# Kernel tuning notes

Hardware: AMD Instinct MI355X
Metric: run time of the kernel (lower is better)

## Reference

```python
import jax, jax.numpy as jnp
import numpy as np

N = 50000
E = 800000
IN_C, HID, OUT_C, DEPTH, HEADS = 3, 128, 64, 4, 4
EPS = 1e-6
NEG_SLOPE = 0.2  # PyG GATConv default leaky_relu slope


def setup_inputs() -> dict:
    key = jax.random.key(0)
    ks = jax.random.split(key, 12)
    x = jax.random.normal(ks[0], (N, IN_C), dtype=jnp.float32)
    edge_index = jax.random.randint(ks[1], (2, E), 0, N, dtype=jnp.int32)
    s = 0.05
    return {
        "x": x,
        "edge_index": edge_index,
        "W_in": jax.random.normal(ks[2], (IN_C, HID), dtype=jnp.float32) * s,
        "b_in": jnp.zeros((HID,), jnp.float32),
        # per-layer GATConv params, stacked over depth
        "W_conv": jax.random.normal(ks[3], (DEPTH, HID, HEADS * HID), dtype=jnp.float32) * s,
        "att_src": jax.random.normal(ks[4], (DEPTH, HEADS, HID), dtype=jnp.float32) * s,
        "att_dst": jax.random.normal(ks[5], (DEPTH, HEADS, HID), dtype=jnp.float32) * s,
        "b_conv": jnp.zeros((DEPTH, HID), jnp.float32),
        "ln_gamma": jnp.ones((DEPTH, HID), jnp.float32),
        "ln_beta": jnp.zeros((DEPTH, HID), jnp.float32),
        "W_out": jax.random.normal(ks[6], (HID, OUT_C), dtype=jnp.float32) * s,
        "b_out": jnp.zeros((OUT_C,), jnp.float32),
    }


def _layer_norm(x, gamma, beta):
    mu = jnp.mean(x, axis=-1, keepdims=True)
    var = jnp.mean(jnp.square(x - mu), axis=-1, keepdims=True)
    return (x - mu) * jax.lax.rsqrt(var + EPS) * gamma + beta


def _gat_conv(x, src, dst, W, a_src, a_dst, bias):
    # x: [N, HID]; src/dst: [E2] (self-loops already appended)
    xh = (x @ W).reshape(N, HEADS, HID)                       # [N, H, C]
    alpha_s = jnp.einsum("nhc,hc->nh", xh, a_src)             # [N, H]
    alpha_d = jnp.einsum("nhc,hc->nh", xh, a_dst)             # [N, H]
    e = jax.nn.leaky_relu(alpha_s[src] + alpha_d[dst], NEG_SLOPE)  # [E2, H]
    # segment softmax over incoming edges of each destination node
    m = jax.ops.segment_max(e, dst, num_segments=N)           # [N, H]
    p = jnp.exp(e - m[dst])                                   # [E2, H]
    z = jax.ops.segment_sum(p, dst, num_segments=N)           # [N, H]
    alpha = p / z[dst]                                        # [E2, H]
    msg = alpha[:, :, None] * xh[src]                         # [E2, H, C]
    out = jax.ops.segment_sum(msg, dst, num_segments=N)       # [N, H, C]
    # concat=False -> mean over heads, then bias
    return out.mean(axis=1) + bias


def reference(x, edge_index, W_in, b_in, W_conv, att_src, att_dst, b_conv,
              ln_gamma, ln_beta, W_out, b_out):
    # add self-loops (PyG GATConv default add_self_loops=True)
    loops = jnp.arange(N, dtype=edge_index.dtype)
    src = jnp.concatenate([edge_index[0], loops])
    dst = jnp.concatenate([edge_index[1], loops])

    h = x @ W_in + b_in
    for i in range(DEPTH):
        residual = h
        h = _layer_norm(h, ln_gamma[i], ln_beta[i])
        h = _gat_conv(h, src, dst, W_conv[i], att_src[i], att_dst[i], b_conv[i])
        h = jax.nn.relu(h)
        h = h + residual
    return h @ W_out + b_out
```

## Files before the change

### kernel.cpp

```cpp
#include <hip/hip_runtime.h>
#include <hip/hip_fp16.h>
#include <math.h>

#define N_NODES 50000
#define E_EDGES 800000
#define E2 (E_EDGES + N_NODES)
#define HID 128
#define HEADS 4
#define OUTC 64
#define DEPTH 4
#define NEG_SLOPE 0.2f
#define LN_EPS 1e-6f
#define NT2 3125
#define AROW 520

typedef float f32x4 __attribute__((ext_vector_type(4)));
typedef float f32x2 __attribute__((ext_vector_type(2)));
typedef _Float16 half8 __attribute__((ext_vector_type(8)));


__global__ void k_deg(const int* __restrict__ ei, int* __restrict__ deg) {
    int e = blockIdx.x * 256 + threadIdx.x;
    if (e >= E2) return;
    int d = (e < E_EDGES) ? ei[E_EDGES + e] : (e - E_EDGES);
    atomicAdd(&deg[d], 1);
}


__global__ __launch_bounds__(256) void k_hist(const int* __restrict__ deg,
                                              int* __restrict__ hist) {
    __shared__ int lh[256];
    int t = threadIdx.x;
    lh[t] = 0;
    __syncthreads();
    int base = blockIdx.x * 1024;
    #pragma unroll
    for (int i = 0; i < 4; ++i) {
        int n = base + t + i * 256;
        if (n < N_NODES) atomicAdd(&lh[min(deg[n], 255)], 1);
    }
    __syncthreads();
    if (lh[t]) atomicAdd(&hist[t], lh[t]);
}


__global__ void k_hscan(const int* __restrict__ hist, int* __restrict__ hcur,
                        int* __restrict__ nprefix, int* __restrict__ eprefix,
                        int* __restrict__ row_ptr) {
    __shared__ int sm[256], se[256];
    int t = threadIdx.x;
    int v = hist[t];
    sm[t] = v;
    se[t] = v * t;
    __syncthreads();
    for (int off = 1; off < 256; off <<= 1) {
        int u = (t >= off) ? sm[t - off] : 0;
        int w = (t >= off) ? se[t - off] : 0;
        __syncthreads();
        sm[t] += u;
        se[t] += w;
        __syncthreads();
    }
    int np = sm[t] - v;
    int ep = se[t] - v * t;
    hcur[t] = np;
    nprefix[t] = np;
    eprefix[t] = ep;
    if (t == 0) row_ptr[N_NODES] = E2;
}


__global__ __launch_bounds__(256) void k_permfill(const int* __restrict__ deg,
                                                  int* __restrict__ hcur,
                                                  const int* __restrict__ nprefix,
                                                  const int* __restrict__ eprefix,
                                                  int* __restrict__ perm,
                                                  int* __restrict__ inv,
                                                  int* __restrict__ row_ptr) {
    __shared__ int lh[256];
    __shared__ int lbase[256];
    int t = threadIdx.x;
    lh[t] = 0;
    __syncthreads();
    int base = blockIdx.x * 1024;
    int myb[4], myr[4];
    #pragma unroll
    for (int i = 0; i < 4; ++i) {
        int n = base + t + i * 256;
        if (n < N_NODES) {
            int b = min(deg[n], 255);
            myb[i] = b;
            myr[i] = atomicAdd(&lh[b], 1);
        } else myb[i] = -1;
    }
    __syncthreads();
    if (lh[t]) lbase[t] = atomicAdd(&hcur[t], lh[t]);
    __syncthreads();
    #pragma unroll
    for (int i = 0; i < 4; ++i) {
        if (myb[i] >= 0) {
            int n = base + t + i * 256;
            int b = myb[i];
            int pos = lbase[b] + myr[i];
            perm[pos] = n;
            inv[n] = pos;
            row_ptr[pos] = eprefix[b] + (pos - nprefix[b]) * b;
        }
    }
}

__global__ void k_fill(const int* __restrict__ ei, const int* __restrict__ row_ptr,
                       const int* __restrict__ inv, int* __restrict__ cur,
                       int* __restrict__ csr_src) {
    int e = blockIdx.x * 256 + threadIdx.x;
    if (e >= E2) return;
    int s, d;
    if (e < E_EDGES) { s = ei[e]; d = ei[E_EDGES + e]; } else { s = d = e - E_EDGES; }
    int nd = inv[d], ns = inv[s];
    int pos = atomicAdd(&cur[nd], 1);
    csr_src[row_ptr[nd] + pos] = ns;
}


__global__ void k_prep(const float* __restrict__ W_conv, const float* __restrict__ att_s,
                       const float* __restrict__ att_d, const float* __restrict__ W_out,
                       _Float16* __restrict__ Bp, float* __restrict__ ws_all,
                       _Float16* __restrict__ Bout) {
    int idx = blockIdx.x * 256 + threadIdx.x;
    if (idx < DEPTH * 65536) {
        int jj    = idx & 7;
        int lane  = (idx >> 3) & 63;
        int kc    = (idx >> 9) & 15;
        int ntile = (idx >> 13) & 7;
        int layer = idx >> 16;
        int k = kc * 32 + (lane >> 4) * 8 + jj;
        int n = ntile * 16 + (lane & 15);
        int hh = k >> 7;
        int s  = k & 127;
        int c  = (s & 7) * 16 + (s >> 3);
        Bp[idx] = (_Float16)(0.25f * W_conv[(size_t)layer * 65536 + (size_t)c * 512 + hh * HID + n]);
        return;
    }
    int i2 = idx - DEPTH * 65536;
    if (i2 < DEPTH * 1024) {
        int j = i2 & 7, c = (i2 >> 3) & 127, layer = i2 >> 10;
        int hh = j & 3, sd = j >> 2;
        const float* Wr = W_conv + (size_t)layer * 65536 + (size_t)c * 512 + hh * HID;
        const float* at = (sd ? att_d : att_s) + (size_t)layer * HEADS * HID + hh * HID;
        float s = 0.f;
        for (int cc = 0; cc < HID; ++cc) s += Wr[cc] * at[cc];
        ws_all[i2] = s;
        return;
    }
    int i3 = i2 - DEPTH * 1024;
    if (i3 < 8192) {
        int j    = i3 & 7;
        int lane = (i3 >> 3) & 63;
        int nt   = (i3 >> 9) & 3;
        int kc   = i3 >> 11;
        int k = kc * 32 + (lane >> 4) * 8 + j;
        int c = (k & 7) * 16 + (k >> 3);
        int n = nt * 16 + (lane & 15);
        Bout[i3] = (_Float16)W_out[(size_t)c * OUTC + n];
    }
}


__global__ __launch_bounds__(256) void k_in_proj_ln(const float* __restrict__ x,
                                                    const int* __restrict__ perm,
                                                    const float* __restrict__ W,
                                                    const float* __restrict__ bias,
                                                    const float* __restrict__ gamma,
                                                    const float* __restrict__ beta,
                                                    const float* __restrict__ ws,
                                                    float* __restrict__ h,
                                                    unsigned char* __restrict__ ln8,
                                                    float* __restrict__ as_,
                                                    float* __restrict__ ad_) {
    int tid = threadIdx.x;
    int lane = tid & 63;
    int nd = blockIdx.x * 4 + (tid >> 6);
    int orig = perm[nd];
    const float* xr = x + (size_t)orig * 3;
    float x0 = xr[0], x1 = xr[1], x2 = xr[2];
    int j0 = lane, j1 = lane + 64;
    float a = bias[j0] + x0 * W[j0] + x1 * W[HID + j0] + x2 * W[2 * HID + j0];
    float b = bias[j1] + x0 * W[j1] + x1 * W[HID + j1] + x2 * W[2 * HID + j1];
    size_t base = (size_t)nd * HID;
    h[base + j0] = a;
    h[base + j1] = b;
    float s = a + b;
    for (int o = 1; o < 64; o <<= 1) s += __shfl_xor(s, o);
    float mu = s * (1.0f / 128.0f);
    float da = a - mu, db = b - mu;
    float v = da * da + db * db;
    for (int o = 1; o < 64; o <<= 1) v += __shfl_xor(v, o);
    float rstd = rsqrtf(v * (1.0f / 128.0f) + LN_EPS);
    float va = da * rstd * gamma[j0] + beta[j0];
    float vb = db * rstd * gamma[j1] + beta[j1];

    float ap[8];
    for (int j = 0; j < 8; ++j)
        ap[j] = va * ws[j0 * 8 + j] + vb * ws[j1 * 8 + j];
    for (int o = 1; o < 64; o <<= 1)
        for (int j = 0; j < 8; ++j) ap[j] += __shfl_xor(ap[j], o);
    if (lane == 0) {
        for (int hh = 0; hh < 4; ++hh) {
            as_[nd * 4 + hh] = ap[hh];
            ad_[nd * 4 + hh] = ap[4 + hh];
        }
    }

    float pv[8];
    for (int t = 0; t < 8; ++t) {
        int c = t * 16 + (lane & 15);
        float s1 = __shfl(va, c & 63);
        float s2 = __shfl(vb, c & 63);
        pv[t] = (c < 64) ? s1 : s2;
    }
    if (lane < 16) {
        int w0 = __builtin_amdgcn_cvt_pk_fp8_f32(pv[0], pv[1], 0, false);
        w0     = __builtin_amdgcn_cvt_pk_fp8_f32(pv[2], pv[3], w0, true);
        int w1 = __builtin_amdgcn_cvt_pk_fp8_f32(pv[4], pv[5], 0, false);
        w1     = __builtin_amdgcn_cvt_pk_fp8_f32(pv[6], pv[7], w1, true);
        *(int2*)(ln8 + base + lane * 8) = make_int2(w0, w1);
    }
}


__global__ __launch_bounds__(256, 4) void k_layer(const unsigned char* __restrict__ ln8r,
                                               const int* __restrict__ row_ptr,
                                               const int* __restrict__ csr_src,
                                               const float* __restrict__ asr,
                                               const float* __restrict__ adr,
                                               const _Float16* __restrict__ Bp,
                                               const float* __restrict__ ws,
                                               const float* __restrict__ bias,
                                               const float* __restrict__ gamma,
                                               const float* __restrict__ beta,
                                               float* __restrict__ h,
                                               unsigned char* __restrict__ ln8w,
                                               float* __restrict__ asw,
                                               float* __restrict__ adw,
                                               const _Float16* __restrict__ Bout,
                                               const int* __restrict__ perm,
                                               const float* __restrict__ bout,
                                               float* __restrict__ out,
                                               int write_ln, int last) {
    __shared__ __align__(16) unsigned char smraw[16 * AROW * 2];
    _Float16* Afr = (_Float16*)smraw;
    float (*Cts)[132] = (float (*)[132])smraw;
    _Float16* Hfr = (_Float16*)(smraw + 8448);

    int tid  = threadIdx.x;
    int lane = tid & 63;
    int w    = tid >> 6;
    int g    = lane >> 4;
    int l    = lane & 15;
    int quad = lane >> 4;
    int l15  = lane & 15;
    int tile = blockIdx.x;
    int m    = w * 4 + g;
    int nd   = tile * 16 + m;

    int e0 = row_ptr[nd], e1 = row_ptr[nd + 1];
    float4 ad4 = *(const float4*)(adr + (size_t)nd * 4);

    f32x2 a00 = (f32x2)(0.f), a01 = (f32x2)(0.f), a02 = (f32x2)(0.f), a03 = (f32x2)(0.f);
    f32x2 a10 = (f32x2)(0.f), a11 = (f32x2)(0.f), a12 = (f32x2)(0.f), a13 = (f32x2)(0.f);
    f32x2 a20 = (f32x2)(0.f), a21 = (f32x2)(0.f), a22 = (f32x2)(0.f), a23 = (f32x2)(0.f);
    f32x2 a30 = (f32x2)(0.f), a31 = (f32x2)(0.f), a32 = (f32x2)(0.f), a33 = (f32x2)(0.f);
    float4 zz = make_float4(0.f, 0.f, 0.f, 0.f);

    const unsigned char* xb = ln8r + l * 8;

#define EDGE_P(Q, P) do {                                                   \
    float t_;                                                               \
    t_ = (Q).x + ad4.x; t_ = (t_ >= 0.f) ? t_ : NEG_SLOPE * t_; (P).x = __expf(t_); \
    t_ = (Q).y + ad4.y; t_ = (t_ >= 0.f) ? t_ : NEG_SLOPE * t_; (P).y = __expf(t_); \
    t_ = (Q).z + ad4.z; t_ = (t_ >= 0.f) ? t_ : NEG_SLOPE * t_; (P).z = __expf(t_); \
    t_ = (Q).w + ad4.w; t_ = (t_ >= 0.f) ? t_ : NEG_SLOPE * t_; (P).w = __expf(t_); \
} while (0)

#define ACC_EDGE(P, X) do {                                                 \
    f32x2 v0 = __builtin_amdgcn_cvt_pk_f32_fp8((X).x, false);               \
    f32x2 v1 = __builtin_amdgcn_cvt_pk_f32_fp8((X).x, true);                \
    f32x2 v2 = __builtin_amdgcn_cvt_pk_f32_fp8((X).y, false);               \
    f32x2 v3 = __builtin_amdgcn_cvt_pk_f32_fp8((X).y, true);                \
    a00 += (f32x2)((P).x) * v0; a01 += (f32x2)((P).x) * v1;                 \
    a02 += (f32x2)((P).x) * v2; a03 += (f32x2)((P).x) * v3;                 \
    a10 += (f32x2)((P).y) * v0; a11 += (f32x2)((P).y) * v1;                 \
    a12 += (f32x2)((P).y) * v2; a13 += (f32x2)((P).y) * v3;                 \
    a20 += (f32x2)((P).z) * v0; a21 += (f32x2)((P).z) * v1;                 \
    a22 += (f32x2)((P).z) * v2; a23 += (f32x2)((P).z) * v3;                 \
    a30 += (f32x2)((P).w) * v0; a31 += (f32x2)((P).w) * v1;                 \
    a32 += (f32x2)((P).w) * v2; a33 += (f32x2)((P).w) * v3;                 \
    zz.x += (P).x; zz.y += (P).y; zz.z += (P).z; zz.w += (P).w;             \
} while (0)

    int e = e0;
    for (; e + 4 <= e1; e += 4) {
        int s0 = csr_src[e];
        int s1 = csr_src[e + 1];
        int s2 = csr_src[e + 2];
        int s3 = csr_src[e + 3];
        float4 q0 = *(const float4*)(asr + (size_t)s0 * 4);
        float4 q1 = *(const float4*)(asr + (size_t)s1 * 4);
        float4 q2 = *(const float4*)(asr + (size_t)s2 * 4);
        float4 q3 = *(const float4*)(asr + (size_t)s3 * 4);
        int2 x0 = *(const int2*)(xb + (size_t)s0 * 128);
        int2 x1 = *(const int2*)(xb + (size_t)s1 * 128);
        int2 x2 = *(const int2*)(xb + (size_t)s2 * 128);
        int2 x3 = *(const int2*)(xb + (size_t)s3 * 128);
        float4 p0, p1, p2, p3;
        EDGE_P(q0, p0);
        EDGE_P(q1, p1);
        EDGE_P(q2, p2);
        EDGE_P(q3, p3);
        ACC_EDGE(p0, x0);
        ACC_EDGE(p1, x1);
        ACC_EDGE(p2, x2);
        ACC_EDGE(p3, x3);
    }
    for (; e < e1; ++e) {
        int s0 = csr_src[e];
        float4 q0 = *(const float4*)(asr + (size_t)s0 * 4);
        int2 x0 = *(const int2*)(xb + (size_t)s0 * 128);
        float4 p0;
        EDGE_P(q0, p0);
        ACC_EDGE(p0, x0);
    }
#undef EDGE_P
#undef ACC_EDGE

    {
        f32x2 i0 = (f32x2)(1.0f / zz.x), i1 = (f32x2)(1.0f / zz.y);
        f32x2 i2 = (f32x2)(1.0f / zz.z), i3 = (f32x2)(1.0f / zz.w);
        a00 *= i0; a01 *= i0; a02 *= i0; a03 *= i0;
        a10 *= i1; a11 *= i1; a12 *= i1; a13 *= i1;
        a20 *= i2; a21 *= i2; a22 *= i2; a23 *= i2;
        a30 *= i3; a31 *= i3; a32 *= i3; a33 *= i3;
        _Float16* rowp = Afr + m * AROW + l15 * 8;
        union { _Float16 hx[8]; int4 v4; } cf;
#define STORE_HEAD(H, P0, P1, P2, P3) do {                                  \
        cf.hx[0] = (_Float16)P0[0]; cf.hx[1] = (_Float16)P0[1];             \
        cf.hx[2] = (_Float16)P1[0]; cf.hx[3] = (_Float16)P1[1];             \
        cf.hx[4] = (_Float16)P2[0]; cf.hx[5] = (_Float16)P2[1];             \
        cf.hx[6] = (_Float16)P3[0]; cf.hx[7] = (_Float16)P3[1];             \
        *(int4*)(rowp + (H) * 128) = cf.v4;                                 \
} while (0)
        STORE_HEAD(0, a00, a01, a02, a03);
        STORE_HEAD(1, a10, a11, a12, a13);
        STORE_HEAD(2, a20, a21, a22, a23);
        STORE_HEAD(3, a30, a31, a32, a33);
#undef STORE_HEAD
    }
    __syncthreads();

    f32x4 c0 = (f32x4)(0.f), c1 = (f32x4)(0.f);
    {
        int nt0 = w * 2, nt1 = w * 2 + 1;
        const _Float16* b0p = Bp + (size_t)nt0 * 8192 + lane * 8;
        const _Float16* b1p = Bp + (size_t)nt1 * 8192 + lane * 8;
        const _Float16* ar = Afr + (lane & 15) * AROW + (lane >> 4) * 8;
        #pragma unroll
        for (int kc = 0; kc < 16; ++kc) {
            half8 a  = *(const half8*)(ar + kc * 32);
            half8 b0 = *(const half8*)(b0p + kc * 512);
            half8 b1 = *(const half8*)(b1p + kc * 512);
            c0 = __builtin_amdgcn_mfma_f32_16x16x32_f16(a, b0, c0, 0, 0, 0);
            c1 = __builtin_amdgcn_mfma_f32_16x16x32_f16(a, b1, c1, 0, 0, 0);
        }
    }
    __syncthreads();
    {
        int nt0 = w * 2, nt1 = w * 2 + 1;
        #pragma unroll
        for (int r = 0; r < 4; ++r) {
            Cts[quad * 4 + r][nt0 * 16 + l15] = c0[r];
            Cts[quad * 4 + r][nt1 * 16 + l15] = c1[r];
        }
    }
    __syncthreads();

    int row = quad * 4 + w;
    int node = tile * 16 + row;
    float* hr = h + (size_t)node * HID;

    float rv[8];
    #pragma unroll
    for (int nt = 0; nt < 8; ++nt) {
        float t = Cts[row][nt * 16 + l15] + bias[nt * 16 + l15];
        t = fmaxf(t, 0.f);
        rv[nt] = t + hr[nt * 16 + l15];
    }
    if (!last) {
        #pragma unroll
        for (int nt = 0; nt < 8; ++nt) hr[nt * 16 + l15] = rv[nt];
    } else {
        union { _Float16 hx[8]; int4 v4; } cf;
        #pragma unroll
        for (int nt = 0; nt < 8; ++nt) cf.hx[nt] = (_Float16)rv[nt];
        int kc = l15 >> 2;
        int lf = (l15 & 3) * 16 + row;
        *(int4*)(Hfr + ((kc * 64 + lf) * 8)) = cf.v4;
    }

    if (write_ln) {
        float ga[8], be[8];
        f32x4 wsa[8], wsb[8];
        #pragma unroll
        for (int nt = 0; nt < 8; ++nt) {
            int c = nt * 16 + l15;
            ga[nt] = gamma[c];
            be[nt] = beta[c];
            wsa[nt] = *(const f32x4*)(ws + c * 8);
            wsb[nt] = *(const f32x4*)(ws + c * 8 + 4);
        }
        float s = 0.f;
        #pragma unroll
        for (int nt = 0; nt < 8; ++nt) s += rv[nt];
        s += __shfl_xor(s, 1); s += __shfl_xor(s, 2);
        s += __shfl_xor(s, 4); s += __shfl_xor(s, 8);
        float mu = s * (1.0f / 128.0f);
        float var = 0.f;
        #pragma unroll
        for (int nt = 0; nt < 8; ++nt) { float d = rv[nt] - mu; var += d * d; }
        var += __shfl_xor(var, 1); var += __shfl_xor(var, 2);
        var += __shfl_xor(var, 4); var += __shfl_xor(var, 8);
        float rstd = rsqrtf(var * (1.0f / 128.0f) + LN_EPS);
        float lnv[8];
        #pragma unroll
        for (int nt = 0; nt < 8; ++nt)
            lnv[nt] = (rv[nt] - mu) * rstd * ga[nt] + be[nt];

        float ap[8];
        #pragma unroll
        for (int j = 0; j < 4; ++j) {
            float t0 = 0.f, t1 = 0.f;
            #pragma unroll
            for (int nt = 0; nt < 8; ++nt) {
                t0 += lnv[nt] * wsa[nt][j];
                t1 += lnv[nt] * wsb[nt][j];
            }
            ap[j] = t0;
            ap[4 + j] = t1;
        }
        #pragma unroll
        for (int j = 0; j < 8; ++j) {
            ap[j] += __shfl_xor(ap[j], 1); ap[j] += __shfl_xor(ap[j], 2);
            ap[j] += __shfl_xor(ap[j], 4); ap[j] += __shfl_xor(ap[j], 8);
        }
        if (l15 == 0) {
            for (int hh = 0; hh < 4; ++hh) {
                asw[node * 4 + hh] = ap[hh];
                adw[node * 4 + hh] = ap[4 + hh];
            }
        }

        int w0 = __builtin_amdgcn_cvt_pk_fp8_f32(lnv[0], lnv[1], 0, false);
        w0     = __builtin_amdgcn_cvt_pk_fp8_f32(lnv[2], lnv[3], w0, true);
        int w1 = __builtin_amdgcn_cvt_pk_fp8_f32(lnv[4], lnv[5], 0, false);
        w1     = __builtin_amdgcn_cvt_pk_fp8_f32(lnv[6], lnv[7], w1, true);
        *(int2*)(ln8w + (size_t)node * 128 + l15 * 8) = make_int2(w0, w1);
    }

    if (last) {
        __syncthreads();
        f32x4 acc = (f32x4)(0.f);
        #pragma unroll
        for (int kc2 = 0; kc2 < 4; ++kc2) {
            half8 a  = *(const half8*)(Hfr + (kc2 * 64 + lane) * 8);
            half8 bf = *(const half8*)(Bout + ((size_t)(kc2 * 4 + w) * 64 + lane) * 8);
            acc = __builtin_amdgcn_mfma_f32_16x16x32_f16(a, bf, acc, 0, 0, 0);
        }
        float bo = bout[w * 16 + l15];
        #pragma unroll
        for (int r = 0; r < 4; ++r) {
            int nodeo = perm[tile * 16 + quad * 4 + r];
            out[(size_t)nodeo * OUTC + w * 16 + l15] = acc[r] + bo;
        }
    }
}


extern "C" void kernel_launch(void* const* d_in, const int* in_sizes, int n_in,
                              void* d_out, int out_size, void* d_ws, size_t ws_size,
                              hipStream_t stream) {
    const float* x       = (const float*)d_in[0];
    const int*   ei      = (const int*)d_in[1];
    const float* W_in    = (const float*)d_in[2];
    const float* b_in    = (const float*)d_in[3];
    const float* W_conv  = (const float*)d_in[4];
    const float* att_src = (const float*)d_in[5];
    const float* att_dst = (const float*)d_in[6];
    const float* b_conv  = (const float*)d_in[7];
    const float* ln_g    = (const float*)d_in[8];
    const float* ln_b    = (const float*)d_in[9];
    const float* W_out   = (const float*)d_in[10];
    const float* b_out   = (const float*)d_in[11];
    float* out = (float*)d_out;

    char* ws = (char*)d_ws;
    size_t off = 0;
    auto alloc = [&](size_t bytes) { void* p = ws + off; off = (off + bytes + 255) & ~(size_t)255; return p; };
    float* h            = (float*)alloc((size_t)N_NODES * HID * 4);
    unsigned char* ln8a = (unsigned char*)alloc((size_t)N_NODES * 128);
    unsigned char* ln8b = (unsigned char*)alloc((size_t)N_NODES * 128);
    float* asa          = (float*)alloc((size_t)N_NODES * 4 * 4);
    float* asb          = (float*)alloc((size_t)N_NODES * 4 * 4);
    float* ada          = (float*)alloc((size_t)N_NODES * 4 * 4);
    float* adb          = (float*)alloc((size_t)N_NODES * 4 * 4);
    _Float16* Bp2       = (_Float16*)alloc((size_t)DEPTH * 65536 * 2);
    float* ws_all       = (float*)alloc((size_t)DEPTH * 1024 * 4);
    _Float16* Bout      = (_Float16*)alloc((size_t)8192 * 2);
    int* deg    = (int*)alloc((size_t)N_NODES * 4);
    int* cur    = (int*)alloc((size_t)N_NODES * 4);
    int* hist   = (int*)alloc(256 * 4);
    int* row_ptr= (int*)alloc((size_t)(N_NODES + 1) * 4);
    int* csr    = (int*)alloc((size_t)E2 * 4);
    int* perm   = (int*)alloc((size_t)N_NODES * 4);
    int* inv    = (int*)alloc((size_t)N_NODES * 4);
    int* hcur   = (int*)alloc(256 * 4);
    int* nprefix= (int*)alloc(256 * 4);
    int* eprefix= (int*)alloc(256 * 4);
    (void)ws_size; (void)n_in; (void)in_sizes; (void)out_size;

    size_t zspan = (char*)(hist + 256) - (char*)deg;
    hipMemsetAsync(deg, 0, zspan, stream);

    k_deg<<<(E2 + 255) / 256, 256, 0, stream>>>(ei, deg);
    int nbh = (N_NODES + 1023) / 1024;
    k_hist<<<nbh, 256, 0, stream>>>(deg, hist);
    k_hscan<<<1, 256, 0, stream>>>(hist, hcur, nprefix, eprefix, row_ptr);
    k_permfill<<<nbh, 256, 0, stream>>>(deg, hcur, nprefix, eprefix, perm, inv, row_ptr);
    k_fill<<<(E2 + 255) / 256, 256, 0, stream>>>(ei, row_ptr, inv, cur, csr);

    int prep_total = DEPTH * 65536 + DEPTH * 1024 + 8192;
    k_prep<<<(prep_total + 255) / 256, 256, 0, stream>>>(W_conv, att_src, att_dst, W_out,
                                                         Bp2, ws_all, Bout);

    k_in_proj_ln<<<N_NODES / 4, 256, 0, stream>>>(x, perm, W_in, b_in, ln_g, ln_b, ws_all,
                                                  h, ln8a, asa, ada);

    for (int i = 0; i < DEPTH; ++i) {
        const float* bcp = b_conv + (size_t)i * HID;
        int write_ln = (i + 1 < DEPTH) ? 1 : 0;
        int last = (i + 1 == DEPTH) ? 1 : 0;
        int nl = (i + 1 < DEPTH) ? i + 1 : i;
        const float* gp = ln_g + (size_t)nl * HID;
        const float* bp = ln_b + (size_t)nl * HID;
        const float* wsp = ws_all + (size_t)nl * 1024;

        const unsigned char* l8r = (i & 1) ? ln8b : ln8a;
        unsigned char*       l8w = (i & 1) ? ln8a : ln8b;
        const float* asr = (i & 1) ? asb : asa;
        float*       asw = (i & 1) ? asa : asb;
        const float* adr = (i & 1) ? adb : ada;
        float*       adw = (i & 1) ? ada : adb;

        k_layer<<<NT2, 256, 0, stream>>>(l8r, row_ptr, csr, asr, adr,
                                         Bp2 + (size_t)i * 65536, wsp,
                                         bcp, gp, bp, h, l8w, asw, adw,
                                         Bout, perm, b_out, out, write_ln, last);
    }
}
```

Before: 430.7 us.

## Split each node's edge aggregation across two half-waves with 512-thread blocks

```diff
diff --git a/kernel.cpp b/kernel.cpp
--- a/kernel.cpp
+++ b/kernel.cpp
@@ -228,7 +228,7 @@
 }
 
 
-__global__ __launch_bounds__(256, 4) void k_layer(const unsigned char* __restrict__ ln8r,
+__global__ __launch_bounds__(512, 8) void k_layer(const unsigned char* __restrict__ ln8r,
                                                const int* __restrict__ row_ptr,
                                                const int* __restrict__ csr_src,
                                                const float* __restrict__ asr,
@@ -255,15 +255,18 @@
     int tid  = threadIdx.x;
     int lane = tid & 63;
     int w    = tid >> 6;
-    int g    = lane >> 4;
-    int l    = lane & 15;
+    int sub  = lane >> 5;
+    int es   = (lane >> 4) & 1;
     int quad = lane >> 4;
     int l15  = lane & 15;
+    int l    = l15;
     int tile = blockIdx.x;
-    int m    = w * 4 + g;
+    int m    = w * 2 + sub;
     int nd   = tile * 16 + m;
 
     int e0 = row_ptr[nd], e1 = row_ptr[nd + 1];
+    int cnt = e1 - e0;
+    int n8 = cnt >> 3;
     float4 ad4 = *(const float4*)(adr + (size_t)nd * 4);
 
     f32x2 a00 = (f32x2)(0.f), a01 = (f32x2)(0.f), a02 = (f32x2)(0.f), a03 = (f32x2)(0.f);
@@ -298,12 +301,12 @@
     zz.x += (P).x; zz.y += (P).y; zz.z += (P).z; zz.w += (P).w;             \
 } while (0)
 
-    int e = e0;
-    for (; e + 4 <= e1; e += 4) {
-        int s0 = csr_src[e];
-        int s1 = csr_src[e + 1];
-        int s2 = csr_src[e + 2];
-        int s3 = csr_src[e + 3];
+    for (int i = 0; i < n8; ++i) {
+        int eb = e0 + 8 * i + es * 4;
+        int s0 = csr_src[eb];
+        int s1 = csr_src[eb + 1];
+        int s2 = csr_src[eb + 2];
+        int s3 = csr_src[eb + 3];
         float4 q0 = *(const float4*)(asr + (size_t)s0 * 4);
         float4 q1 = *(const float4*)(asr + (size_t)s1 * 4);
         float4 q2 = *(const float4*)(asr + (size_t)s2 * 4);
@@ -322,18 +325,33 @@
         ACC_EDGE(p2, x2);
         ACC_EDGE(p3, x3);
     }
-    for (; e < e1; ++e) {
-        int s0 = csr_src[e];
-        float4 q0 = *(const float4*)(asr + (size_t)s0 * 4);
-        int2 x0 = *(const int2*)(xb + (size_t)s0 * 128);
-        float4 p0;
-        EDGE_P(q0, p0);
-        ACC_EDGE(p0, x0);
+    {
+        int tb = e0 + 8 * n8 + es * 4;
+        int te = min(tb + 4, e1);
+        for (int e = tb; e < te; ++e) {
+            int s0 = csr_src[e];
+            float4 q0 = *(const float4*)(asr + (size_t)s0 * 4);
+            int2 x0 = *(const int2*)(xb + (size_t)s0 * 128);
+            float4 p0;
+            EDGE_P(q0, p0);
+            ACC_EDGE(p0, x0);
+        }
     }
 #undef EDGE_P
 #undef ACC_EDGE
 
-    {
+#define MRG(v) v[0] += __shfl_xor(v[0], 16); v[1] += __shfl_xor(v[1], 16)
+    MRG(a00); MRG(a01); MRG(a02); MRG(a03);
+    MRG(a10); MRG(a11); MRG(a12); MRG(a13);
+    MRG(a20); MRG(a21); MRG(a22); MRG(a23);
+    MRG(a30); MRG(a31); MRG(a32); MRG(a33);
+#undef MRG
+    zz.x += __shfl_xor(zz.x, 16);
+    zz.y += __shfl_xor(zz.y, 16);
+    zz.z += __shfl_xor(zz.z, 16);
+    zz.w += __shfl_xor(zz.w, 16);
+
+    if (es == 0) {
         f32x2 i0 = (f32x2)(1.0f / zz.x), i1 = (f32x2)(1.0f / zz.y);
         f32x2 i2 = (f32x2)(1.0f / zz.z), i3 = (f32x2)(1.0f / zz.w);
         a00 *= i0; a01 *= i0; a02 *= i0; a03 *= i0;
@@ -357,128 +375,125 @@
     }
     __syncthreads();
 
-    f32x4 c0 = (f32x4)(0.f), c1 = (f32x4)(0.f);
+    f32x4 c0 = (f32x4)(0.f);
     {
-        int nt0 = w * 2, nt1 = w * 2 + 1;
-        const _Float16* b0p = Bp + (size_t)nt0 * 8192 + lane * 8;
-        const _Float16* b1p = Bp + (size_t)nt1 * 8192 + lane * 8;
+        const _Float16* b0p = Bp + (size_t)w * 8192 + lane * 8;
         const _Float16* ar = Afr + (lane & 15) * AROW + (lane >> 4) * 8;
         #pragma unroll
         for (int kc = 0; kc < 16; ++kc) {
             half8 a  = *(const half8*)(ar + kc * 32);
             half8 b0 = *(const half8*)(b0p + kc * 512);
-            half8 b1 = *(const half8*)(b1p + kc * 512);
             c0 = __builtin_amdgcn_mfma_f32_16x16x32_f16(a, b0, c0, 0, 0, 0);
-            c1 = __builtin_amdgcn_mfma_f32_16x16x32_f16(a, b1, c1, 0, 0, 0);
         }
     }
     __syncthreads();
     {
-        int nt0 = w * 2, nt1 = w * 2 + 1;
         #pragma unroll
-        for (int r = 0; r < 4; ++r) {
-            Cts[quad * 4 + r][nt0 * 16 + l15] = c0[r];
-            Cts[quad * 4 + r][nt1 * 16 + l15] = c1[r];
-        }
-    }
-    __syncthreads();
-
-    int row = quad * 4 + w;
-    int node = tile * 16 + row;
-    float* hr = h + (size_t)node * HID;
-
-    float rv[8];
-    #pragma unroll
-    for (int nt = 0; nt < 8; ++nt) {
-        float t = Cts[row][nt * 16 + l15] + bias[nt * 16 + l15];
-        t = fmaxf(t, 0.f);
-        rv[nt] = t + hr[nt * 16 + l15];
-    }
-    if (!last) {
-        #pragma unroll
-        for (int nt = 0; nt < 8; ++nt) hr[nt * 16 + l15] = rv[nt];
-    } else {
-        union { _Float16 hx[8]; int4 v4; } cf;
-        #pragma unroll
-        for (int nt = 0; nt < 8; ++nt) cf.hx[nt] = (_Float16)rv[nt];
-        int kc = l15 >> 2;
-        int lf = (l15 & 3) * 16 + row;
-        *(int4*)(Hfr + ((kc * 64 + lf) * 8)) = cf.v4;
-    }
-
-    if (write_ln) {
-        float ga[8], be[8];
-        f32x4 wsa[8], wsb[8];
+        for (int r = 0; r < 4; ++r)
+            Cts[quad * 4 + r][w * 16 + l15] = c0[r];
+    }
+    __syncthreads();
+
+    if (w < 4) {
+        int row = quad * 4 + w;
+        int node = tile * 16 + row;
+        float* hr = h + (size_t)node * HID;
+
+        float rv[8];
         #pragma unroll
         for (int nt = 0; nt < 8; ++nt) {
-            int c = nt * 16 + l15;
-            ga[nt] = gamma[c];
-            be[nt] = beta[c];
-            wsa[nt] = *(const f32x4*)(ws + c * 8);
-            wsb[nt] = *(const f32x4*)(ws + c * 8 + 4);
-        }
-        float s = 0.f;
-        #pragma unroll
-        for (int nt = 0; nt < 8; ++nt) s += rv[nt];
-        s += __shfl_xor(s, 1); s += __shfl_xor(s, 2);
-        s += __shfl_xor(s, 4); s += __shfl_xor(s, 8);
-        float mu = s * (1.0f / 128.0f);
-        float var = 0.f;
-        #pragma unroll
-        for (int nt = 0; nt < 8; ++nt) { float d = rv[nt] - mu; var += d * d; }
-        var += __shfl_xor(var, 1); var += __shfl_xor(var, 2);
-        var += __shfl_xor(var, 4); var += __shfl_xor(var, 8);
-        float rstd = rsqrtf(var * (1.0f / 128.0f) + LN_EPS);
-        float lnv[8];
-        #pragma unroll
-        for (int nt = 0; nt < 8; ++nt)
-            lnv[nt] = (rv[nt] - mu) * rstd * ga[nt] + be[nt];
-
-        float ap[8];
-        #pragma unroll
-        for (int j = 0; j < 4; ++j) {
-            float t0 = 0.f, t1 = 0.f;
+            float t = Cts[row][nt * 16 + l15] + bias[nt * 16 + l15];
+            t = fmaxf(t, 0.f);
+            rv[nt] = t + hr[nt * 16 + l15];
+        }
+        if (!last) {
+            #pragma unroll
+            for (int nt = 0; nt < 8; ++nt) hr[nt * 16 + l15] = rv[nt];
+        } else {
+            union { _Float16 hx[8]; int4 v4; } cf;
+            #pragma unroll
+            for (int nt = 0; nt < 8; ++nt) cf.hx[nt] = (_Float16)rv[nt];
+            int kc = l15 >> 2;
+            int lf = (l15 & 3) * 16 + row;
+            *(int4*)(Hfr + ((kc * 64 + lf) * 8)) = cf.v4;
+        }
+
+        if (write_ln) {
+            float ga[8], be[8];
+            f32x4 wsa[8], wsb[8];
             #pragma unroll
             for (int nt = 0; nt < 8; ++nt) {
-                t0 += lnv[nt] * wsa[nt][j];
-                t1 += lnv[nt] * wsb[nt][j];
+                int c = nt * 16 + l15;
+                ga[nt] = gamma[c];
+                be[nt] = beta[c];
+                wsa[nt] = *(const f32x4*)(ws + c * 8);
+                wsb[nt] = *(const f32x4*)(ws + c * 8 + 4);
             }
-            ap[j] = t0;
-            ap[4 + j] = t1;
-        }
-        #pragma unroll
-        for (int j = 0; j < 8; ++j) {
-            ap[j] += __shfl_xor(ap[j], 1); ap[j] += __shfl_xor(ap[j], 2);
-            ap[j] += __shfl_xor(ap[j], 4); ap[j] += __shfl_xor(ap[j], 8);
-        }
-        if (l15 == 0) {
-            for (int hh = 0; hh < 4; ++hh) {
-                asw[node * 4 + hh] = ap[hh];
-                adw[node * 4 + hh] = ap[4 + hh];
+            float s = 0.f;
+            #pragma unroll
+            for (int nt = 0; nt < 8; ++nt) s += rv[nt];
+            s += __shfl_xor(s, 1); s += __shfl_xor(s, 2);
+            s += __shfl_xor(s, 4); s += __shfl_xor(s, 8);
+            float mu = s * (1.0f / 128.0f);
+            float var = 0.f;
+            #pragma unroll
+            for (int nt = 0; nt < 8; ++nt) { float d = rv[nt] - mu; var += d * d; }
+            var += __shfl_xor(var, 1); var += __shfl_xor(var, 2);
+            var += __shfl_xor(var, 4); var += __shfl_xor(var, 8);
+            float rstd = rsqrtf(var * (1.0f / 128.0f) + LN_EPS);
+            float lnv[8];
+            #pragma unroll
+            for (int nt = 0; nt < 8; ++nt)
+                lnv[nt] = (rv[nt] - mu) * rstd * ga[nt] + be[nt];
+
+            float ap[8];
+            #pragma unroll
+            for (int j = 0; j < 4; ++j) {
+                float t0 = 0.f, t1 = 0.f;
+                #pragma unroll
+                for (int nt = 0; nt < 8; ++nt) {
+                    t0 += lnv[nt] * wsa[nt][j];
+                    t1 += lnv[nt] * wsb[nt][j];
+                }
+                ap[j] = t0;
+                ap[4 + j] = t1;
             }
-        }
-
-        int w0 = __builtin_amdgcn_cvt_pk_fp8_f32(lnv[0], lnv[1], 0, false);
-        w0     = __builtin_amdgcn_cvt_pk_fp8_f32(lnv[2], lnv[3], w0, true);
-        int w1 = __builtin_amdgcn_cvt_pk_fp8_f32(lnv[4], lnv[5], 0, false);
-        w1     = __builtin_amdgcn_cvt_pk_fp8_f32(lnv[6], lnv[7], w1, true);
-        *(int2*)(ln8w + (size_t)node * 128 + l15 * 8) = make_int2(w0, w1);
+            #pragma unroll
+            for (int j = 0; j < 8; ++j) {
+                ap[j] += __shfl_xor(ap[j], 1); ap[j] += __shfl_xor(ap[j], 2);
+                ap[j] += __shfl_xor(ap[j], 4); ap[j] += __shfl_xor(ap[j], 8);
+            }
+            if (l15 == 0) {
+                for (int hh2 = 0; hh2 < 4; ++hh2) {
+                    asw[node * 4 + hh2] = ap[hh2];
+                    adw[node * 4 + hh2] = ap[4 + hh2];
+                }
+            }
+
+            int w0 = __builtin_amdgcn_cvt_pk_fp8_f32(lnv[0], lnv[1], 0, false);
+            w0     = __builtin_amdgcn_cvt_pk_fp8_f32(lnv[2], lnv[3], w0, true);
+            int w1 = __builtin_amdgcn_cvt_pk_fp8_f32(lnv[4], lnv[5], 0, false);
+            w1     = __builtin_amdgcn_cvt_pk_fp8_f32(lnv[6], lnv[7], w1, true);
+            *(int2*)(ln8w + (size_t)node * 128 + l15 * 8) = make_int2(w0, w1);
+        }
     }
 
     if (last) {
         __syncthreads();
-        f32x4 acc = (f32x4)(0.f);
-        #pragma unroll
-        for (int kc2 = 0; kc2 < 4; ++kc2) {
-            half8 a  = *(const half8*)(Hfr + (kc2 * 64 + lane) * 8);
-            half8 bf = *(const half8*)(Bout + ((size_t)(kc2 * 4 + w) * 64 + lane) * 8);
-            acc = __builtin_amdgcn_mfma_f32_16x16x32_f16(a, bf, acc, 0, 0, 0);
-        }
-        float bo = bout[w * 16 + l15];
-        #pragma unroll
-        for (int r = 0; r < 4; ++r) {
-            int nodeo = perm[tile * 16 + quad * 4 + r];
-            out[(size_t)nodeo * OUTC + w * 16 + l15] = acc[r] + bo;
+        if (w < 4) {
+            f32x4 acc = (f32x4)(0.f);
+            #pragma unroll
+            for (int kc2 = 0; kc2 < 4; ++kc2) {
+                half8 a  = *(const half8*)(Hfr + (kc2 * 64 + lane) * 8);
+                half8 bf = *(const half8*)(Bout + ((size_t)(kc2 * 4 + w) * 64 + lane) * 8);
+                acc = __builtin_amdgcn_mfma_f32_16x16x32_f16(a, bf, acc, 0, 0, 0);
+            }
+            float bo = bout[w * 16 + l15];
+            #pragma unroll
+            for (int r = 0; r < 4; ++r) {
+                int nodeo = perm[tile * 16 + quad * 4 + r];
+                out[(size_t)nodeo * OUTC + w * 16 + l15] = acc[r] + bo;
+            }
         }
     }
 }
@@ -559,7 +574,7 @@
         const float* adr = (i & 1) ? adb : ada;
         float*       adw = (i & 1) ? ada : adb;
 
-        k_layer<<<NT2, 256, 0, stream>>>(l8r, row_ptr, csr, asr, adr,
+        k_layer<<<NT2, 512, 0, stream>>>(l8r, row_ptr, csr, asr, adr,
                                          Bp2 + (size_t)i * 65536, wsp,
                                          bcp, gp, bp, h, l8w, asw, adw,
                                          Bout, perm, b_out, out, write_ln, last);
```

Measured after the change: 884.8 us. +105.4%, slower.
